# Kernel tuning notes

Hardware: AMD Instinct MI355X
Metric: run time of the kernel (lower is better)

The kernel has to match this reference:

```python
import jax, jax.numpy as jnp
import numpy as np

COMMITMENT_COST = 0.25
NUM_CODEBOOKS = 8192
EMBED_DIM = 256


def setup_inputs() -> dict:
    key = jax.random.key(0)
    kx, kc = jax.random.split(key)
    x = jax.random.normal(kx, (64, 512, 256), dtype=jnp.float32)
    codebook = jax.random.normal(kc, (NUM_CODEBOOKS, EMBED_DIM), dtype=jnp.float32)
    return {"x": x, "codebook": codebook, "hidden_dim": EMBED_DIM}


def reference(x, codebook, hidden_dim):
    # Flatten tokens: [N, D]
    flat = x.reshape(-1, hidden_dim)
    # Squared L2 distances to every codebook entry: [N, K]
    distances = (
        jnp.sum(flat * flat, axis=1, keepdims=True)
        + jnp.sum(codebook * codebook, axis=1)
        - 2.0 * jnp.matmul(flat, codebook.T)
    )
    encoding_indices = jnp.argmin(distances, axis=1)  # [N]
    quantized = jnp.take(codebook, encoding_indices, axis=0).reshape(x.shape)
    # Commitment loss (codebook detached -> plain MSE here in fwd)
    commitment_loss = COMMITMENT_COST * jnp.mean((quantized - x) ** 2)
    # Straight-through estimator
    quantized = x + jax.lax.stop_gradient(quantized - x)
    return quantized, commitment_loss
```

## Files before the change

### kernel.cpp

```cpp
#include <hip/hip_runtime.h>
#include <math.h>

#define N_TOK 32768
#define DDIM  256
#define KCB   8192
#define SLICES 4
#define KS     (KCB / SLICES)
#define TCODES 64
#define NSTEP  (KS / TCODES)
#define MARGIN 1.0f
#define NFBLK  (N_TOK / 4)

typedef _Float16 half_t;
typedef half_t half8 __attribute__((ext_vector_type(8)));
typedef half_t half4 __attribute__((ext_vector_type(4)));
typedef float  f32x4 __attribute__((ext_vector_type(4)));
typedef float  f32x2 __attribute__((ext_vector_type(2)));

#define GLOBAL_AS __attribute__((address_space(1)))
#define LDS_AS    __attribute__((address_space(3)))

__global__ __launch_bounds__(64) void prep_cb(const float* __restrict__ cb,
                                              half_t* __restrict__ cb16,
                                              float* __restrict__ cnorm) {
    int code = blockIdx.x;
    int lane = threadIdx.x;
    f32x4 v = *(const f32x4*)(cb + (size_t)code * DDIM + lane * 4);
    half4 h; h[0]=(half_t)v[0]; h[1]=(half_t)v[1]; h[2]=(half_t)v[2]; h[3]=(half_t)v[3];
    *(half4*)(cb16 + (size_t)code * DDIM + lane * 4) = h;
    float s = v[0]*v[0] + v[1]*v[1] + v[2]*v[2] + v[3]*v[3];
    #pragma unroll
    for (int off = 32; off > 0; off >>= 1) s += __shfl_down(s, off);
    if (lane == 0) cnorm[code] = s;
}

__device__ __forceinline__ half8 ldcvt8(const float* __restrict__ p) {
    f32x4 a = *(const f32x4*)p;
    f32x4 b = *(const f32x4*)(p + 4);
    half8 h;
    h[0]=(half_t)a[0]; h[1]=(half_t)a[1]; h[2]=(half_t)a[2]; h[3]=(half_t)a[3];
    h[4]=(half_t)b[0]; h[5]=(half_t)b[1]; h[6]=(half_t)b[2]; h[7]=(half_t)b[3];
    return h;
}

__device__ __forceinline__ float packkey(float a, unsigned code) {
    return __uint_as_float((__float_as_uint(a) & 0xFFFFE000u) | code);
}

__global__ __launch_bounds__(256, 2)
void passA(const float* __restrict__ x, const half_t* __restrict__ cb16,
           const float* __restrict__ cnorm, float* __restrict__ cand) {

    __shared__ __align__(16) half_t buf[2][TCODES * 256];

    const int tid  = threadIdx.x;
    const int w    = tid >> 6;
    const int lane = tid & 63;
    const int quad = lane >> 4;
    const int mcol = lane & 15;
    const int tokBase   = blockIdx.x * 256 + w * 64;
    const int codeBase0 = blockIdx.y * KS;

    half8 afrag[4][8];
    #pragma unroll
    for (int rt = 0; rt < 4; rt++) {
        const float* xr = x + (size_t)(tokBase + rt * 16 + mcol) * DDIM + quad * 8;
        #pragma unroll
        for (int dk = 0; dk < 8; dk++)
            afrag[rt][dk] = ldcvt8(xr + dk * 32);
    }

    int boff[8];
    #pragma unroll
    for (int dk = 0; dk < 8; dk++)
        boff[dk] = mcol * 256 + (((dk * 4 + quad) ^ (mcol & 7)) * 8);

    float k0[4][4], k1[4][4];
    #pragma unroll
    for (int rt = 0; rt < 4; rt++)
        #pragma unroll
        for (int r = 0; r < 4; r++) { k0[rt][r] = -INFINITY; k1[rt][r] = -INFINITY; }

    const char* cbbase = (const char*)(cb16 + (size_t)codeBase0 * DDIM);
    #define STAGE(nt, b)                                                        \
        {                                                                       \
            const char* srcb = cbbase + (size_t)(nt) * (TCODES * 512);          \
            _Pragma("unroll")                                                   \
            for (int o = 0; o < 8; o++) {                                       \
                int L = o * 256 + tid;                                          \
                int r = L >> 5, c = (L & 31) ^ (r & 7);                         \
                __builtin_amdgcn_global_load_lds(                               \
                    (const GLOBAL_AS void*)(srcb + r * 512 + c * 16),           \
                    (LDS_AS void*)&buf[b][(o * 256 + w * 64) * 8], 16, 0, 0);   \
            }                                                                   \
        }

    STAGE(0, 0)
    __syncthreads();

    for (int nt = 0; nt < NSTEP; nt++) {
        if (nt + 1 < NSTEP) STAGE(nt + 1, (nt + 1) & 1)

        const half_t* cur = buf[nt & 1];
        const int codeBase = codeBase0 + nt * TCODES;

        #pragma unroll
        for (int p = 0; p < 2; p++) {
            const float mc0 = -0.5f * cnorm[codeBase + p * 32 + mcol];
            const float mc1 = -0.5f * cnorm[codeBase + p * 32 + 16 + mcol];
            f32x4 acc[2][4];
            #pragma unroll
            for (int rt = 0; rt < 4; rt++) {
                acc[0][rt][0]=mc0; acc[0][rt][1]=mc0; acc[0][rt][2]=mc0; acc[0][rt][3]=mc0;
                acc[1][rt][0]=mc1; acc[1][rt][1]=mc1; acc[1][rt][2]=mc1; acc[1][rt][3]=mc1;
            }
            const half_t* crow0 = cur + (p * 32) * 256;
            const half_t* crow1 = cur + (p * 32 + 16) * 256;
            #pragma unroll
            for (int dk = 0; dk < 8; dk++) {
                half8 bf0 = *(const half8*)(crow0 + boff[dk]);
                half8 bf1 = *(const half8*)(crow1 + boff[dk]);
                #pragma unroll
                for (int rt = 0; rt < 4; rt++) {
                    acc[0][rt] = __builtin_amdgcn_mfma_f32_16x16x32_f16(afrag[rt][dk], bf0, acc[0][rt], 0, 0, 0);
                    acc[1][rt] = __builtin_amdgcn_mfma_f32_16x16x32_f16(afrag[rt][dk], bf1, acc[1][rt], 0, 0, 0);
                }
            }
            const unsigned code0 = (unsigned)(codeBase + p * 32 + mcol);
            const unsigned code1 = code0 + 16;
            #pragma unroll
            for (int rt = 0; rt < 4; rt++)
                #pragma unroll
                for (int r = 0; r < 4; r++) {
                    float a = packkey(acc[0][rt][r], code0);
                    float b = packkey(acc[1][rt][r], code1);
                    k1[rt][r] = fmaxf(k1[rt][r], __builtin_amdgcn_fmed3f(k0[rt][r], a, b));
                    k0[rt][r] = fmaxf(fmaxf(k0[rt][r], a), b);
                }
        }
        __syncthreads();
    }

    #pragma unroll
    for (int s = 1; s < 16; s <<= 1) {
        #pragma unroll
        for (int rt = 0; rt < 4; rt++)
            #pragma unroll
            for (int r = 0; r < 4; r++) {
                float o0 = __shfl_xor(k0[rt][r], s, 64);
                float o1 = __shfl_xor(k1[rt][r], s, 64);
                float n1 = fmaxf(fminf(k0[rt][r], o0), fmaxf(k1[rt][r], o1));
                k0[rt][r] = fmaxf(k0[rt][r], o0);
                k1[rt][r] = n1;
            }
    }
    if (mcol == 0) {
        #pragma unroll
        for (int rt = 0; rt < 4; rt++)
            #pragma unroll
            for (int r = 0; r < 4; r++) {
                int token = tokBase + rt * 16 + quad * 4 + r;
                f32x2 kk; kk[0] = k0[rt][r]; kk[1] = k1[rt][r];
                *(f32x2*)&cand[(size_t)token * (SLICES * 2) + blockIdx.y * 2] = kk;
            }
    }
}

__global__ __launch_bounds__(256) void finalize_kernel(
    const float* __restrict__ x, const float* __restrict__ cb,
    const float* __restrict__ cnorm, const float* __restrict__ cand,
    float* __restrict__ out, float* __restrict__ partials) {

    const int tid = threadIdx.x, w = tid >> 6, lane = tid & 63;
    const int token = blockIdx.x * 4 + w;
    const float* xrow = x + (size_t)token * DDIM;

    f32x4 ka = *(const f32x4*)(cand + (size_t)token * 8);
    f32x4 kb = *(const f32x4*)(cand + (size_t)token * 8 + 4);
    float v[8] = {ka[0], ka[1], ka[2], ka[3], kb[0], kb[1], kb[2], kb[3]};
    float t0 = -INFINITY, t1 = -INFINITY;
    #pragma unroll
    for (int j = 0; j < 8; j++) {
        float m = fminf(t0, v[j]);
        t0 = fmaxf(t0, v[j]);
        t1 = fmaxf(t1, m);
    }
    int bidx = (int)(__float_as_uint(t0) & 0x1FFFu);

    if (!(t0 - t1 > MARGIN)) {
        const int j = lane >> 3, sub = lane & 7;
        int cj = (int)(__float_as_uint(v[j]) & 0x1FFFu);
        const float* crow = cb + (size_t)cj * DDIM;
        float p = 0.0f;
        #pragma unroll
        for (int c = 0; c < 8; c++) {
            f32x4 xa = *(const f32x4*)(xrow + c * 32 + sub * 4);
            f32x4 ca = *(const f32x4*)(crow + c * 32 + sub * 4);
            p += xa[0]*ca[0] + xa[1]*ca[1] + xa[2]*ca[2] + xa[3]*ca[3];
        }
        p += __shfl_xor(p, 1, 64);
        p += __shfl_xor(p, 2, 64);
        p += __shfl_xor(p, 4, 64);
        float bd = cnorm[cj] - 2.0f * p;
        int   bi = cj;
        #pragma unroll
        for (int s = 8; s < 64; s <<= 1) {
            float od = __shfl_xor(bd, s, 64);
            int   oi = __shfl_xor(bi, s, 64);
            if (od < bd || (od == bd && oi < bi)) { bd = od; bi = oi; }
        }
        bidx = bi;
    }

    f32x4 cv = *(const f32x4*)(cb + (size_t)bidx * DDIM + lane * 4);
    f32x4 xv = *(const f32x4*)(xrow + lane * 4);
    *(f32x4*)(out + (size_t)token * DDIM + lane * 4) = cv;
    float d0 = cv[0]-xv[0], d1 = cv[1]-xv[1], d2 = cv[2]-xv[2], d3 = cv[3]-xv[3];
    float lsum = d0*d0 + d1*d1 + d2*d2 + d3*d3;

    __shared__ float red[256];
    red[tid] = lsum;
    __syncthreads();
    #pragma unroll
    for (int s = 128; s > 0; s >>= 1) {
        if (tid < s) red[tid] += red[tid + s];
        __syncthreads();
    }
    if (tid == 0) partials[blockIdx.x] = red[0];
}

__global__ __launch_bounds__(256) void reduce_loss(const float* __restrict__ partials,
                                                   float* __restrict__ out) {
    const int tid = threadIdx.x;
    float s = 0.0f;
    #pragma unroll
    for (int i = 0; i < 8; i++) {
        f32x4 v = *(const f32x4*)(partials + (size_t)(i * 256 + tid) * 4);
        s += v[0] + v[1] + v[2] + v[3];
    }
    __shared__ float red[256];
    red[tid] = s;
    __syncthreads();
    #pragma unroll
    for (int st = 128; st > 0; st >>= 1) {
        if (tid < st) red[tid] += red[tid + st];
        __syncthreads();
    }
    if (tid == 0)
        out[(size_t)N_TOK * DDIM] = red[0] * (0.25f / (float)((size_t)N_TOK * DDIM));
}

extern "C" void kernel_launch(void* const* d_in, const int* in_sizes, int n_in,
                              void* d_out, int out_size, void* d_ws, size_t ws_size,
                              hipStream_t stream) {
    const float* x  = (const float*)d_in[0];
    const float* cb = (const float*)d_in[1];
    float* out = (float*)d_out;

    half_t* cb16     = (half_t*)d_ws;
    float*  cnorm    = (float*)(cb16 + (size_t)KCB * DDIM);
    float*  cand     = cnorm + KCB;
    float*  partials = cand + (size_t)N_TOK * 8;

    prep_cb<<<KCB, 64, 0, stream>>>(cb, cb16, cnorm);
    dim3 gA(N_TOK / 256, SLICES);
    passA<<<gA, 256, 0, stream>>>(x, cb16, cnorm, cand);
    finalize_kernel<<<NFBLK, 256, 0, stream>>>(x, cb, cnorm, cand, out, partials);
    reduce_loss<<<1, 256, 0, stream>>>(partials, out);
}
```

Before: 224.1 us.

## Load codebook tiles directly into registers, dropping LDS staging in distance pass

```diff
diff --git a/kernel.cpp b/kernel.cpp
--- a/kernel.cpp
+++ b/kernel.cpp
@@ -6,8 +6,9 @@
 #define KCB   8192
 #define SLICES 4
 #define KS     (KCB / SLICES)
-#define TCODES 64
+#define TCODES 16
 #define NSTEP  (KS / TCODES)
+#define TOKW   64
 #define MARGIN 1.0f
 #define NFBLK  (N_TOK / 4)
 
@@ -16,9 +17,6 @@
 typedef half_t half4 __attribute__((ext_vector_type(4)));
 typedef float  f32x4 __attribute__((ext_vector_type(4)));
 typedef float  f32x2 __attribute__((ext_vector_type(2)));
-
-#define GLOBAL_AS __attribute__((address_space(1)))
-#define LDS_AS    __attribute__((address_space(3)))
 
 __global__ __launch_bounds__(64) void prep_cb(const float* __restrict__ cb,
                                               half_t* __restrict__ cb16,
@@ -43,22 +41,20 @@
     return h;
 }
 
-__device__ __forceinline__ float packkey(float a, unsigned code) {
-    return __uint_as_float((__float_as_uint(a) & 0xFFFFE000u) | code);
-}
-
-__global__ __launch_bounds__(256, 2)
+__device__ __forceinline__ float packkey(unsigned mask, unsigned code, float a) {
+    float r;
+    asm("v_bfi_b32 %0, %1, %2, %3" : "=v"(r) : "s"(mask), "v"(code), "v"(a));
+    return r;
+}
+
+__global__ __launch_bounds__(64, 2)
 void passA(const float* __restrict__ x, const half_t* __restrict__ cb16,
            const float* __restrict__ cnorm, float* __restrict__ cand) {
 
-    __shared__ __align__(16) half_t buf[2][TCODES * 256];
-
-    const int tid  = threadIdx.x;
-    const int w    = tid >> 6;
-    const int lane = tid & 63;
+    const int lane = threadIdx.x & 63;
     const int quad = lane >> 4;
     const int mcol = lane & 15;
-    const int tokBase   = blockIdx.x * 256 + w * 64;
+    const int tokBase   = blockIdx.x * TOKW;
     const int codeBase0 = blockIdx.y * KS;
 
     half8 afrag[4][8];
@@ -70,75 +66,62 @@
             afrag[rt][dk] = ldcvt8(xr + dk * 32);
     }
 
-    int boff[8];
-    #pragma unroll
-    for (int dk = 0; dk < 8; dk++)
-        boff[dk] = mcol * 256 + (((dk * 4 + quad) ^ (mcol & 7)) * 8);
-
     float k0[4][4], k1[4][4];
     #pragma unroll
     for (int rt = 0; rt < 4; rt++)
         #pragma unroll
         for (int r = 0; r < 4; r++) { k0[rt][r] = -INFINITY; k1[rt][r] = -INFINITY; }
 
-    const char* cbbase = (const char*)(cb16 + (size_t)codeBase0 * DDIM);
-    #define STAGE(nt, b)                                                        \
+    const half_t* bbase = cb16 + (size_t)(codeBase0 + mcol) * DDIM + quad * 8;
+    const float*  cnp   = cnorm + codeBase0 + mcol;
+
+    const unsigned kmask = 0x1FFFu;
+    unsigned codev = (unsigned)(codeBase0 + mcol);
+
+    #define LOADT(B, CN, nt_)                                                   \
         {                                                                       \
-            const char* srcb = cbbase + (size_t)(nt) * (TCODES * 512);          \
-            _Pragma("unroll")                                                   \
-            for (int o = 0; o < 8; o++) {                                       \
-                int L = o * 256 + tid;                                          \
-                int r = L >> 5, c = (L & 31) ^ (r & 7);                         \
-                __builtin_amdgcn_global_load_lds(                               \
-                    (const GLOBAL_AS void*)(srcb + r * 512 + c * 16),           \
-                    (LDS_AS void*)&buf[b][(o * 256 + w * 64) * 8], 16, 0, 0);   \
+            const half_t* bp = bbase + (size_t)(nt_) * (TCODES * DDIM);         \
+            _Pragma("unroll")                                                   \
+            for (int dk = 0; dk < 8; dk++)                                      \
+                B[dk] = *(const half8*)(bp + dk * 32);                          \
+            CN = cnp[(nt_) * TCODES];                                           \
+        }
+
+    #define COMPUTE(B, CN)                                                      \
+        {                                                                       \
+            const float mc = -0.5f * (CN);                                      \
+            f32x4 acc[4];                                                       \
+            _Pragma("unroll")                                                   \
+            for (int rt = 0; rt < 4; rt++) {                                    \
+                acc[rt][0]=mc; acc[rt][1]=mc; acc[rt][2]=mc; acc[rt][3]=mc;     \
             }                                                                   \
-        }
-
-    STAGE(0, 0)
-    __syncthreads();
-
-    for (int nt = 0; nt < NSTEP; nt++) {
-        if (nt + 1 < NSTEP) STAGE(nt + 1, (nt + 1) & 1)
-
-        const half_t* cur = buf[nt & 1];
-        const int codeBase = codeBase0 + nt * TCODES;
-
-        #pragma unroll
-        for (int p = 0; p < 2; p++) {
-            const float mc0 = -0.5f * cnorm[codeBase + p * 32 + mcol];
-            const float mc1 = -0.5f * cnorm[codeBase + p * 32 + 16 + mcol];
-            f32x4 acc[2][4];
-            #pragma unroll
-            for (int rt = 0; rt < 4; rt++) {
-                acc[0][rt][0]=mc0; acc[0][rt][1]=mc0; acc[0][rt][2]=mc0; acc[0][rt][3]=mc0;
-                acc[1][rt][0]=mc1; acc[1][rt][1]=mc1; acc[1][rt][2]=mc1; acc[1][rt][3]=mc1;
-            }
-            const half_t* crow0 = cur + (p * 32) * 256;
-            const half_t* crow1 = cur + (p * 32 + 16) * 256;
-            #pragma unroll
-            for (int dk = 0; dk < 8; dk++) {
-                half8 bf0 = *(const half8*)(crow0 + boff[dk]);
-                half8 bf1 = *(const half8*)(crow1 + boff[dk]);
-                #pragma unroll
-                for (int rt = 0; rt < 4; rt++) {
-                    acc[0][rt] = __builtin_amdgcn_mfma_f32_16x16x32_f16(afrag[rt][dk], bf0, acc[0][rt], 0, 0, 0);
-                    acc[1][rt] = __builtin_amdgcn_mfma_f32_16x16x32_f16(afrag[rt][dk], bf1, acc[1][rt], 0, 0, 0);
-                }
-            }
-            const unsigned code0 = (unsigned)(codeBase + p * 32 + mcol);
-            const unsigned code1 = code0 + 16;
-            #pragma unroll
-            for (int rt = 0; rt < 4; rt++)
-                #pragma unroll
-                for (int r = 0; r < 4; r++) {
-                    float a = packkey(acc[0][rt][r], code0);
-                    float b = packkey(acc[1][rt][r], code1);
-                    k1[rt][r] = fmaxf(k1[rt][r], __builtin_amdgcn_fmed3f(k0[rt][r], a, b));
-                    k0[rt][r] = fmaxf(fmaxf(k0[rt][r], a), b);
-                }
-        }
-        __syncthreads();
+            __builtin_amdgcn_s_setprio(1);                                      \
+            _Pragma("unroll")                                                   \
+            for (int dk = 0; dk < 8; dk++)                                      \
+                _Pragma("unroll")                                               \
+                for (int rt = 0; rt < 4; rt++)                                  \
+                    acc[rt] = __builtin_amdgcn_mfma_f32_16x16x32_f16(           \
+                        afrag[rt][dk], B[dk], acc[rt], 0, 0, 0);                \
+            __builtin_amdgcn_s_setprio(0);                                      \
+            _Pragma("unroll")                                                   \
+            for (int rt = 0; rt < 4; rt++)                                      \
+                _Pragma("unroll")                                               \
+                for (int r = 0; r < 4; r++) {                                   \
+                    float a = packkey(kmask, codev, acc[rt][r]);                \
+                    k1[rt][r] = __builtin_amdgcn_fmed3f(k0[rt][r], a, k1[rt][r]); \
+                    k0[rt][r] = fmaxf(k0[rt][r], a);                            \
+                }                                                               \
+            codev += TCODES;                                                    \
+        }
+
+    half8 Bp[8], Bq[8];
+    float cnpv, cnqv;
+    LOADT(Bp, cnpv, 0)
+    for (int nt = 0; nt < NSTEP; nt += 2) {
+        LOADT(Bq, cnqv, nt + 1)
+        COMPUTE(Bp, cnpv)
+        if (nt + 2 < NSTEP) LOADT(Bp, cnpv, nt + 2)
+        COMPUTE(Bq, cnqv)
     }
 
     #pragma unroll
@@ -189,20 +172,23 @@
 
     if (!(t0 - t1 > MARGIN)) {
         const int j = lane >> 3, sub = lane & 7;
-        int cj = (int)(__float_as_uint(v[j]) & 0x1FFFu);
-        const float* crow = cb + (size_t)cj * DDIM;
-        float p = 0.0f;
-        #pragma unroll
-        for (int c = 0; c < 8; c++) {
-            f32x4 xa = *(const f32x4*)(xrow + c * 32 + sub * 4);
-            f32x4 ca = *(const f32x4*)(crow + c * 32 + sub * 4);
-            p += xa[0]*ca[0] + xa[1]*ca[1] + xa[2]*ca[2] + xa[3]*ca[3];
-        }
-        p += __shfl_xor(p, 1, 64);
-        p += __shfl_xor(p, 2, 64);
-        p += __shfl_xor(p, 4, 64);
-        float bd = cnorm[cj] - 2.0f * p;
+        int   cj = (int)(__float_as_uint(v[j]) & 0x1FFFu);
+        float bd = INFINITY;
         int   bi = cj;
+        if (v[j] >= t0 - MARGIN) {
+            const float* crow = cb + (size_t)cj * DDIM;
+            float p = 0.0f;
+            #pragma unroll
+            for (int c = 0; c < 8; c++) {
+                f32x4 xa = *(const f32x4*)(xrow + c * 32 + sub * 4);
+                f32x4 ca = *(const f32x4*)(crow + c * 32 + sub * 4);
+                p += xa[0]*ca[0] + xa[1]*ca[1] + xa[2]*ca[2] + xa[3]*ca[3];
+            }
+            p += __shfl_xor(p, 1, 64);
+            p += __shfl_xor(p, 2, 64);
+            p += __shfl_xor(p, 4, 64);
+            bd = cnorm[cj] - 2.0f * p;
+        }
         #pragma unroll
         for (int s = 8; s < 64; s <<= 1) {
             float od = __shfl_xor(bd, s, 64);
@@ -263,8 +249,8 @@
     float*  partials = cand + (size_t)N_TOK * 8;
 
     prep_cb<<<KCB, 64, 0, stream>>>(cb, cb16, cnorm);
-    dim3 gA(N_TOK / 256, SLICES);
-    passA<<<gA, 256, 0, stream>>>(x, cb16, cnorm, cand);
+    dim3 gA(N_TOK / TOKW, SLICES);
+    passA<<<gA, 64, 0, stream>>>(x, cb16, cnorm, cand);
     finalize_kernel<<<NFBLK, 256, 0, stream>>>(x, cb, cnorm, cand, out, partials);
     reduce_loss<<<1, 256, 0, stream>>>(partials, out);
 }
```

Result: slower. 404.9 us (+80.7%).
